# Performance work log

Hardware: AMD Instinct MI355X
Metric: run time of the kernel (lower is better)

## Reference

```python
import jax, jax.numpy as jnp
import numpy as np

B, T, D = 2, 2048, 2048
H, KVH, DH = 16, 4, 128
WINDOW = 1024
EPS = 1e-6
THETA = 10000.0

def _rmsnorm(x, eps=EPS):
    # RMSNorm over last dim, no affine (rmsnorm_weights=False)
    return x * jax.lax.rsqrt(jnp.mean(jnp.square(x), axis=-1, keepdims=True) + eps)

def _rope_tables(seq_len, dim, theta):
    inv_freq = 1.0 / theta ** (jnp.arange(0, dim, 2, dtype=jnp.float32) / dim)
    t = jnp.arange(seq_len, dtype=jnp.float32)
    freqs = jnp.outer(t, inv_freq)  # [T, dim//2]
    return jnp.cos(freqs), jnp.sin(freqs)

def _apply_rotary(x, cos, sin):
    # x: [B,T,H,DH]; cos/sin: [T, DH//2] broadcast to [1,T,1,DH//2]
    d = x.shape[-1] // 2
    x1, x2 = x[..., :d], x[..., d:]
    c = cos[None, :, None, :]
    s = sin[None, :, None, :]
    y1 = x1 * c + x2 * s
    y2 = -x1 * s + x2 * c
    return jnp.concatenate([y1, y2], axis=-1)

def setup_inputs() -> dict:
    key = jax.random.key(0)
    ks = jax.random.split(key, 5)
    sc = 0.02
    return {
        "hidden_states": jax.random.normal(ks[0], (B, T, D), dtype=jnp.float32),
        "Wq": jax.random.normal(ks[1], (D, H * DH), dtype=jnp.float32) * sc,
        "Wk": jax.random.normal(ks[2], (D, KVH * DH), dtype=jnp.float32) * sc,
        "Wv": jax.random.normal(ks[3], (D, KVH * DH), dtype=jnp.float32) * sc,
        "Wg": jax.random.normal(ks[4], (D, D), dtype=jnp.float32) * sc,
        "softmax_scaler": jnp.ones((H,), dtype=jnp.float32),
        "gn_weight": jnp.ones((DH,), dtype=jnp.float32),
    }

def reference(hidden_states, Wq, Wk, Wv, Wg, softmax_scaler, gn_weight):
    x = hidden_states
    b, t, _ = x.shape
    q = (x @ Wq).reshape(b, t, H, DH)
    k = (x @ Wk).reshape(b, t, KVH, DH)
    v = (x @ Wv).reshape(b, t, KVH, DH)

    # per-head QK RMSNorm
    q = _rmsnorm(q)
    k = _rmsnorm(k)

    # RoPE (local / swa branch, base=rope_theta_local)
    cos, sin = _rope_tables(t, DH, THETA)
    q = _apply_rotary(q, cos, sin)
    k = _apply_rotary(k, cos, sin)

    # scalable softmax: scale q by learned per-head scaler * log(position+1)
    log_pos = jnp.log(jnp.arange(1, t + 1, dtype=jnp.float32))  # [T]
    q = q * (softmax_scaler[None, None, :, None] * log_pos[None, :, None, None])

    # GQA: repeat kv heads (each kv head -> n_rep consecutive q heads)
    n_rep = H // KVH
    k = jnp.repeat(k, n_rep, axis=2)  # [B,T,H,DH]
    v = jnp.repeat(v, n_rep, axis=2)

    # causal + sliding-window attention (flash window_size=(w,w) causal => q-k in [0, w])
    scale = 1.0 / jnp.sqrt(jnp.float32(DH))
    scores = jnp.einsum("bqhd,bkhd->bhqk", q, k) * scale  # [B,H,T,T]
    qi = jnp.arange(t)[:, None]
    ki = jnp.arange(t)[None, :]
    mask = (ki <= qi) & (qi - ki <= WINDOW)  # [T,T]
    scores = jnp.where(mask[None, None, :, :], scores, jnp.float32(-1e30))
    p = jax.nn.softmax(scores, axis=-1)
    y = jnp.einsum("bhqk,bkhd->bqhd", p, v)  # [B,T,H,DH]

    # gate (elementwise, silu) then group RMSNorm (norm_before_gate_attn=False)
    g = (x @ Wg).reshape(b, t, H, DH)
    y = y * jax.nn.silu(g)
    y = _rmsnorm(y) * gn_weight  # groupnorm: RMSNorm over d_head with weight

    return y.reshape(b, t, D)
```

## Files before the change

### kernel.cpp

```cpp
#include <hip/hip_runtime.h>

#define B_   2
#define T_   2048
#define D_   2048
#define H_   16
#define KVH_ 4
#define DH_  128
#define WIN_ 1024
#define N_TOT 5120

typedef __attribute__((ext_vector_type(4))) float    f32x4;
typedef __attribute__((ext_vector_type(8))) _Float16 half8;
typedef __attribute__((ext_vector_type(8))) short    short8;
typedef __attribute__((ext_vector_type(4))) short    short4v;

__device__ __forceinline__ unsigned short f2h(float f) {
    _Float16 h = (_Float16)f;
    return __builtin_bit_cast(unsigned short, h);
}

__device__ __forceinline__ f32x4 mfma16x16x32(short8 a, short8 b, f32x4 c) {
    return __builtin_amdgcn_mfma_f32_16x16x32_f16(
        __builtin_bit_cast(half8, a), __builtin_bit_cast(half8, b), c, 0, 0, 0);
}

__device__ __forceinline__ void glds16(const void* g, void* l) {
    __builtin_amdgcn_global_load_lds(
        (const __attribute__((address_space(1))) unsigned int*)g,
        (__attribute__((address_space(3))) unsigned int*)l, 16, 0, 0);
}

__global__ void rope_tab_kernel(float* __restrict__ cosT, float* __restrict__ sinT) {
    int idx = blockIdx.x * 256 + threadIdx.x;
    if (idx >= T_ * 64) return;
    int t = idx >> 6, i = idx & 63;
    float inv = powf(10000.0f, -(float)i / 64.0f);
    float f = (float)t * inv;
    cosT[idx] = cosf(f);
    sinT[idx] = sinf(f);
}

__global__ void xconv_kernel(const float* __restrict__ xf, unsigned short* __restrict__ xb) {
    int idx = blockIdx.x * 256 + threadIdx.x;
    float4 f0 = ((const float4*)xf)[idx * 2];
    float4 f1 = ((const float4*)xf)[idx * 2 + 1];
    unsigned p0 = f2h(f0.x) | ((unsigned)f2h(f0.y) << 16);
    unsigned p1 = f2h(f0.z) | ((unsigned)f2h(f0.w) << 16);
    unsigned p2 = f2h(f1.x) | ((unsigned)f2h(f1.y) << 16);
    unsigned p3 = f2h(f1.z) | ((unsigned)f2h(f1.w) << 16);
    ((uint4*)xb)[idx] = make_uint4(p0, p1, p2, p3);
}

__global__ __launch_bounds__(256) void wtconv_kernel(
    const float* __restrict__ W, unsigned short* __restrict__ WTdst, int nW) {
    __shared__ unsigned short tile[64][72];
    int ntiles_n = nW >> 6;
    int n0 = (blockIdx.x % ntiles_n) * 64;
    int k0 = (blockIdx.x / ntiles_n) * 64;
    int tid = threadIdx.x;
    {
        int kr = tid >> 2, c0 = (tid & 3) * 16;
        const float* src = W + (size_t)(k0 + kr) * nW + n0 + c0;
        float4 a = ((const float4*)src)[0], b = ((const float4*)src)[1];
        float4 c = ((const float4*)src)[2], d = ((const float4*)src)[3];
        uint4 lo = make_uint4(f2h(a.x) | ((unsigned)f2h(a.y) << 16),
                              f2h(a.z) | ((unsigned)f2h(a.w) << 16),
                              f2h(b.x) | ((unsigned)f2h(b.y) << 16),
                              f2h(b.z) | ((unsigned)f2h(b.w) << 16));
        uint4 hi = make_uint4(f2h(c.x) | ((unsigned)f2h(c.y) << 16),
                              f2h(c.z) | ((unsigned)f2h(c.w) << 16),
                              f2h(d.x) | ((unsigned)f2h(d.y) << 16),
                              f2h(d.z) | ((unsigned)f2h(d.w) << 16));
        *(uint4*)(&tile[kr][c0])     = lo;
        *(uint4*)(&tile[kr][c0 + 8]) = hi;
    }
    __syncthreads();
    {
        int nr = tid >> 2, kc = (tid & 3) * 16;
        unsigned short vals[16];
        #pragma unroll
        for (int j = 0; j < 16; ++j) vals[j] = tile[kc + j][nr];
        uint4 lo = *(uint4*)(&vals[0]);
        uint4 hi = *(uint4*)(&vals[8]);
        unsigned short* dst = WTdst + (size_t)(n0 + nr) * D_ + k0 + kc;
        *(uint4*)(dst)     = lo;
        *(uint4*)(dst + 8) = hi;
    }
}

__global__ __launch_bounds__(256) void gemm_bt_kernel(
    const unsigned short* __restrict__ Ab, const unsigned short* __restrict__ Bt,
    float* __restrict__ C) {
    __shared__ unsigned short As[128 * 64];
    __shared__ unsigned short Bs[128 * 64];
    const int tid = threadIdx.x;
    const int l = tid & 63, w = tid >> 6;
    const int wr = w >> 1, wc = w & 1;
    int swz = (blockIdx.x & 7) * 160 + (blockIdx.x >> 3);
    const int mb0 = (swz / 40) * 128, nb0 = (swz % 40) * 128;

    f32x4 acc[4][4] = {};

    for (int k0 = 0; k0 < D_; k0 += 64) {
        __syncthreads();
        #pragma unroll
        for (int r = 0; r < 4; ++r) {
            int idx = r * 256 + tid;
            int m = idx >> 3, u = idx & 7;
            glds16(Ab + (size_t)(mb0 + m) * D_ + k0 + u * 8, &As[idx * 8]);
            glds16(Bt + (size_t)(nb0 + m) * D_ + k0 + u * 8, &Bs[idx * 8]);
        }
        __syncthreads();
        #pragma unroll
        for (int ks = 0; ks < 2; ++ks) {
            short8 af[4], bfr[4];
            #pragma unroll
            for (int mi = 0; mi < 4; ++mi)
                af[mi] = *(const short8*)(&As[(wr * 64 + mi * 16 + (l & 15)) * 64 + ks * 32 + (l >> 4) * 8]);
            #pragma unroll
            for (int ni = 0; ni < 4; ++ni)
                bfr[ni] = *(const short8*)(&Bs[(wc * 64 + ni * 16 + (l & 15)) * 64 + ks * 32 + (l >> 4) * 8]);
            #pragma unroll
            for (int mi = 0; mi < 4; ++mi)
                #pragma unroll
                for (int ni = 0; ni < 4; ++ni)
                    acc[mi][ni] = mfma16x16x32(af[mi], bfr[ni], acc[mi][ni]);
        }
    }
    #pragma unroll
    for (int mi = 0; mi < 4; ++mi)
        #pragma unroll
        for (int ni = 0; ni < 4; ++ni)
            #pragma unroll
            for (int i = 0; i < 4; ++i)
                C[(size_t)(mb0 + wr * 64 + mi * 16 + (l >> 4) * 4 + i) * N_TOT
                  + nb0 + wc * 64 + ni * 16 + (l & 15)] = acc[mi][ni][i];
}

__global__ __launch_bounds__(256) void qk_post_kernel(
    const float* __restrict__ C, int colofs, unsigned short* __restrict__ dst,
    const float* __restrict__ cosT, const float* __restrict__ sinT,
    const float* __restrict__ sscale, int nheads, int is_q) {
    int rid = blockIdx.x * 4 + (threadIdx.x >> 6);
    int lane = threadIdx.x & 63;
    int h = rid % nheads;
    int t = (rid / nheads) % T_;
    int b = rid / (nheads * T_);
    const float* row = C + (size_t)(b * T_ + t) * N_TOT + colofs + h * 128;
    float x1 = row[lane], x2 = row[lane + 64];
    float ss = x1 * x1 + x2 * x2;
    #pragma unroll
    for (int m = 1; m < 64; m <<= 1) ss += __shfl_xor(ss, m);
    float rn = rsqrtf(ss * (1.0f / 128.0f) + 1e-6f);
    float c = cosT[t * 64 + lane], s = sinT[t * 64 + lane];
    float y1 = x1 * c + x2 * s;
    float y2 = x2 * c - x1 * s;
    float sc = rn;
    if (is_q) sc *= sscale[h] * logf((float)(t + 1)) * 0.08838834764831845f;
    y1 *= sc; y2 *= sc;
    unsigned short* drow = dst + ((size_t)(b * nheads + h) * T_ + t) * 128;
    drow[lane]      = f2h(y1);
    drow[lane + 64] = f2h(y2);
}

__global__ void vconv_kernel(const float* __restrict__ C, unsigned short* __restrict__ vb) {
    int idx = blockIdx.x * 256 + threadIdx.x;
    int c8  = idx & 15;
    int kvh = (idx >> 4) & 3;
    int t   = (idx >> 6) & 2047;
    int b   = idx >> 17;
    const float* src = C + (size_t)(b * T_ + t) * N_TOT + 2560 + kvh * 128 + c8 * 8;
    float4 f0 = ((const float4*)src)[0];
    float4 f1 = ((const float4*)src)[1];
    unsigned p0 = f2h(f0.x) | ((unsigned)f2h(f0.y) << 16);
    unsigned p1 = f2h(f0.z) | ((unsigned)f2h(f0.w) << 16);
    unsigned p2 = f2h(f1.x) | ((unsigned)f2h(f1.y) << 16);
    unsigned p3 = f2h(f1.z) | ((unsigned)f2h(f1.w) << 16);
    unsigned short* dst = vb + ((size_t)(b * KVH_ + kvh) * T_ + t) * 128 + c8 * 8;
    *(uint4*)dst = make_uint4(p0, p1, p2, p3);
}

__global__ __launch_bounds__(256) void attn_kernel(
    const unsigned short* __restrict__ Q, const unsigned short* __restrict__ K,
    const unsigned short* __restrict__ V, float* __restrict__ O) {
    __shared__ __align__(16) char smem[34816];
    unsigned short* Kl = (unsigned short*)smem;
    unsigned short* Vt = (unsigned short*)smem + 64 * 136;

    const int tid = threadIdx.x, l = tid & 63, w = tid >> 6;
    const int qbi = blockIdx.x & 31, h = (blockIdx.x >> 5) & 15, b = blockIdx.x >> 9;
    const int qb = qbi * 64, kvh = h >> 2;
    const unsigned short* Qp = Q + (size_t)(b * H_ + h) * T_ * 128;
    const unsigned short* Kp = K + (size_t)(b * KVH_ + kvh) * T_ * 128;
    const unsigned short* Vp = V + (size_t)(b * KVH_ + kvh) * T_ * 128;
    const int qw = qb + w * 16;
    const int qi = qw + (l & 15);

    short8 qfr[4];
    #pragma unroll
    for (int dk = 0; dk < 4; ++dk)
        qfr[dk] = *(const short8*)(Qp + (size_t)(qw + (l & 15)) * 128 + dk * 32 + (l >> 4) * 8);

    f32x4 Oa[8] = {};
    float mrun = -1e30f, lrun = 0.0f;

    const int k0 = (qb - WIN_ > 0) ? (qb - WIN_) : 0;
    for (int tile = k0; tile <= qb; tile += 64) {
        __syncthreads();
        #pragma unroll
        for (int r = 0; r < 4; ++r) {
            int uidx = tid + 256 * r;
            int key = uidx >> 4, u = uidx & 15;
            int4 val = *(const int4*)(Kp + (size_t)(tile + key) * 128 + u * 8);
            int byte = (key * 256 + u * 16) ^ ((key & 7) << 4);
            *(int4*)((char*)Kl + byte) = val;
        }
        {
            int kb = tid >> 4, db = tid & 15;
            unsigned short vr[4][8];
            #pragma unroll
            for (int ki = 0; ki < 4; ++ki)
                *(int4*)vr[ki] = *(const int4*)(Vp + (size_t)(tile + kb * 4 + ki) * 128 + db * 8);
            #pragma unroll
            for (int di = 0; di < 8; ++di) {
                unsigned lo = vr[0][di] | ((unsigned)vr[1][di] << 16);
                unsigned hi = vr[2][di] | ((unsigned)vr[3][di] << 16);
                *(uint2*)(&Vt[(db * 8 + di) * 68 + kb * 4]) = make_uint2(lo, hi);
            }
        }
        __syncthreads();

        #pragma unroll
        for (int pair = 0; pair < 2; ++pair) {
            int kp = tile + pair * 32;
            if (kp > qw + 15) continue;
            if (kp + 31 < qw - WIN_) continue;

            f32x4 s0 = {}, s1 = {};
            __builtin_amdgcn_s_setprio(1);
            #pragma unroll
            for (int dk = 0; dk < 4; ++dk) {
                int r0 = pair * 32 + (l & 15), r1 = r0 + 16;
                int c  = dk * 64 + (l >> 4) * 16;
                short8 kf0 = *(const short8*)((char*)Kl + ((r0 * 256 + c) ^ ((r0 & 7) << 4)));
                short8 kf1 = *(const short8*)((char*)Kl + ((r1 * 256 + c) ^ ((r1 & 7) << 4)));
                s0 = mfma16x16x32(kf0, qfr[dk], s0);
                s1 = mfma16x16x32(kf1, qfr[dk], s1);
            }
            __builtin_amdgcn_s_setprio(0);
            float smax = -1e30f;
            #pragma unroll
            for (int i = 0; i < 4; ++i) {
                int ki0 = kp + (l >> 4) * 4 + i;
                int ki1 = ki0 + 16;
                if (ki0 > qi || qi - ki0 > WIN_) s0[i] = -1e30f;
                if (ki1 > qi || qi - ki1 > WIN_) s1[i] = -1e30f;
                smax = fmaxf(smax, fmaxf(s0[i], s1[i]));
            }
            smax = fmaxf(smax, __shfl_xor(smax, 16));
            smax = fmaxf(smax, __shfl_xor(smax, 32));
            if (!__all(smax <= mrun + 8.0f)) {
                float mnew = fmaxf(mrun, smax);
                float alpha = __expf(mrun - mnew);
                lrun *= alpha;
                #pragma unroll
                for (int dt = 0; dt < 8; ++dt) Oa[dt] *= alpha;
                mrun = mnew;
            }
            float psum = 0.0f;
            short8 pb;
            #pragma unroll
            for (int i = 0; i < 4; ++i) {
                float p0 = __expf(s0[i] - mrun);
                float p1 = __expf(s1[i] - mrun);
                psum += p0 + p1;
                pb[i]     = (short)f2h(p0);
                pb[i + 4] = (short)f2h(p1);
            }
            psum += __shfl_xor(psum, 16);
            psum += __shfl_xor(psum, 32);
            lrun += psum;
            __builtin_amdgcn_s_setprio(1);
            #pragma unroll
            for (int dt = 0; dt < 8; ++dt) {
                union { short4v hlf[2]; short8 v8; } vu;
                vu.hlf[0] = *(const short4v*)(&Vt[(dt * 16 + (l & 15)) * 68 + pair * 32 +      (l >> 4) * 4]);
                vu.hlf[1] = *(const short4v*)(&Vt[(dt * 16 + (l & 15)) * 68 + pair * 32 + 16 + (l >> 4) * 4]);
                Oa[dt] = mfma16x16x32(vu.v8, pb, Oa[dt]);
            }
            __builtin_amdgcn_s_setprio(0);
        }
    }

    __syncthreads();
    float* Ow = (float*)smem + w * (16 * 132);
    float inv = 1.0f / lrun;
    #pragma unroll
    for (int dt = 0; dt < 8; ++dt)
        #pragma unroll
        for (int i = 0; i < 4; ++i)
            Ow[(l & 15) * 132 + dt * 16 + (l >> 4) * 4 + i] = Oa[dt][i] * inv;
    #pragma unroll
    for (int j = 0; j < 8; ++j) {
        int idx4 = l + 64 * j;
        int row = idx4 >> 5, dpos = (idx4 & 31) * 4;
        float4 val = *(const float4*)(&Ow[row * 132 + dpos]);
        *(float4*)(O + ((size_t)(b * H_ + h) * T_ + qw + row) * 128 + dpos) = val;
    }
}

__global__ __launch_bounds__(256) void gate_norm_kernel(
    const float* __restrict__ o, const float* __restrict__ C,
    const float* __restrict__ gnw, float* __restrict__ out) {
    int rid = blockIdx.x * 4 + (threadIdx.x >> 6);
    int lane = threadIdx.x & 63;
    int h = rid & 15;
    int t = (rid >> 4) & 2047;
    int b = rid >> 15;
    const float* orow = o + ((size_t)(b * H_ + h) * T_ + t) * 128;
    const float* grow = C + (size_t)(b * T_ + t) * N_TOT + 3072 + h * 128;
    float o1 = orow[lane], o2 = orow[lane + 64];
    float g1 = grow[lane], g2 = grow[lane + 64];
    float y1 = o1 * (g1 / (1.0f + __expf(-g1)));
    float y2 = o2 * (g2 / (1.0f + __expf(-g2)));
    float ss = y1 * y1 + y2 * y2;
    #pragma unroll
    for (int m = 1; m < 64; m <<= 1) ss += __shfl_xor(ss, m);
    float rn = rsqrtf(ss * (1.0f / 128.0f) + 1e-6f);
    float* wrow = out + (size_t)rid * 128;
    wrow[lane]      = y1 * rn * gnw[lane];
    wrow[lane + 64] = y2 * rn * gnw[lane + 64];
}

extern "C" void kernel_launch(void* const* d_in, const int* in_sizes, int n_in,
                              void* d_out, int out_size, void* d_ws, size_t ws_size,
                              hipStream_t stream) {
    const float* x      = (const float*)d_in[0];
    const float* Wq     = (const float*)d_in[1];
    const float* Wk     = (const float*)d_in[2];
    const float* Wv     = (const float*)d_in[3];
    const float* Wg     = (const float*)d_in[4];
    const float* sscale = (const float*)d_in[5];
    const float* gnw    = (const float*)d_in[6];
    float* out = (float*)d_out;

    char* ws = (char*)d_ws;
    unsigned short* xh16 = (unsigned short*)(ws);
    unsigned short* WT   = (unsigned short*)(ws + 16777216);
    float*          C    = (float*)(ws + 37748736);
    unsigned short* qh16 = (unsigned short*)(ws + 121634816);
    unsigned short* kh16 = (unsigned short*)(ws + 138412032);
    unsigned short* vh16 = (unsigned short*)(ws + 142606336);
    float*          cosT = (float*)(ws + 146800640);
    float*          sinT = (float*)(ws + 147324928);
    float*          o    = (float*)(ws);

    rope_tab_kernel<<<512, 256, 0, stream>>>(cosT, sinT);

    xconv_kernel<<<4096, 256, 0, stream>>>(x, xh16);
    wtconv_kernel<<<1024, 256, 0, stream>>>(Wq, WT,                       2048);
    wtconv_kernel<<<256,  256, 0, stream>>>(Wk, WT + (size_t)2048 * D_,   512);
    wtconv_kernel<<<256,  256, 0, stream>>>(Wv, WT + (size_t)2560 * D_,   512);
    wtconv_kernel<<<1024, 256, 0, stream>>>(Wg, WT + (size_t)3072 * D_,   2048);

    gemm_bt_kernel<<<1280, 256, 0, stream>>>(xh16, WT, C);

    qk_post_kernel<<<16384, 256, 0, stream>>>(C, 0,    qh16, cosT, sinT, sscale, H_,   1);
    qk_post_kernel<<<4096,  256, 0, stream>>>(C, 2048, kh16, cosT, sinT, sscale, KVH_, 0);
    vconv_kernel<<<1024, 256, 0, stream>>>(C, vh16);

    attn_kernel<<<B_ * H_ * (T_ / 64), 256, 0, stream>>>(qh16, kh16, vh16, o);

    gate_norm_kernel<<<16384, 256, 0, stream>>>(o, C, gnw, out);
}
```

Measured before the change: 425.1 us.

## Replace fused QKVG GEMM with 256x256 tile, 8-wave double-buffered pipelined kernel

Rewrites the projection GEMM to use 256x256 output tiles with 8 waves per block, split-K LDS staging into double-buffered halves, and explicit interleaving of global-to-LDS prefetch with MFMA clusters using sched/s_barrier and vmcnt waits. The aim is to raise data reuse per loaded tile and hide global-load latency behind matrix math, cutting the GEMM's share of total time. The cost is 128 KB of LDS per block and a larger accumulator register footprint. There are also only 320 blocks for 256 CUs, which may leave a partial wave tail.

Result: faster. 413.0 us (-2.9%).

```diff
diff --git a/kernel.cpp b/kernel.cpp
--- a/kernel.cpp
+++ b/kernel.cpp
@@ -88,53 +88,104 @@
     }
 }
 
-__global__ __launch_bounds__(256) void gemm_bt_kernel(
+#define LDSOFF(d,s,kh) ((((d)*2+(s))*2+(kh))*8192)
+#define LDA_(d,qk,mf) (*(const short8*)(&ldsbuf[LDSOFF(d,0,qk) + (wm*128 + (mf)*16 + lr)*32 + lg*8]))
+#define LDB_(d,qk,nf) (*(const short8*)(&ldsbuf[LDSOFF(d,1,qk) + (wn*64  + (nf)*16 + lr)*32 + lg*8]))
+#define STAGE(d,s,kh,tile,base,R0) do { \
+    _Pragma("unroll") \
+    for (int ll = 0; ll < 2; ++ll) { \
+      int c_ = ll*512 + tid; \
+      int rr_ = c_ >> 2, sl_ = c_ & 3; \
+      glds16((base) + (size_t)((R0) + rr_) * D_ + (tile)*64 + (kh)*32 + sl_*8, \
+             &ldsbuf[LDSOFF(d,s,kh) + c_*8]); \
+    } \
+  } while (0)
+#define SBAR do { __builtin_amdgcn_sched_barrier(0); __builtin_amdgcn_s_barrier(); } while (0)
+#define MFMA_CLUSTER(QN2) do { \
+    __builtin_amdgcn_s_setprio(1); \
+    _Pragma("unroll") \
+    for (int mf = 0; mf < 8; ++mf) { \
+      acc[mf][(QN2)*2]   = mfma16x16x32(af[mf], bf0, acc[mf][(QN2)*2]); \
+      acc[mf][(QN2)*2+1] = mfma16x16x32(af[mf], bf1, acc[mf][(QN2)*2+1]); \
+    } \
+    __builtin_amdgcn_s_setprio(0); \
+  } while (0)
+
+__global__ __launch_bounds__(512, 2) void gemm8_kernel(
     const unsigned short* __restrict__ Ab, const unsigned short* __restrict__ Bt,
     float* __restrict__ C) {
-    __shared__ unsigned short As[128 * 64];
-    __shared__ unsigned short Bs[128 * 64];
+    __shared__ unsigned short ldsbuf[65536];
     const int tid = threadIdx.x;
-    const int l = tid & 63, w = tid >> 6;
-    const int wr = w >> 1, wc = w & 1;
-    int swz = (blockIdx.x & 7) * 160 + (blockIdx.x >> 3);
-    const int mb0 = (swz / 40) * 128, nb0 = (swz % 40) * 128;
-
-    f32x4 acc[4][4] = {};
-
-    for (int k0 = 0; k0 < D_; k0 += 64) {
-        __syncthreads();
-        #pragma unroll
-        for (int r = 0; r < 4; ++r) {
-            int idx = r * 256 + tid;
-            int m = idx >> 3, u = idx & 7;
-            glds16(Ab + (size_t)(mb0 + m) * D_ + k0 + u * 8, &As[idx * 8]);
-            glds16(Bt + (size_t)(nb0 + m) * D_ + k0 + u * 8, &Bs[idx * 8]);
-        }
-        __syncthreads();
-        #pragma unroll
-        for (int ks = 0; ks < 2; ++ks) {
-            short8 af[4], bfr[4];
-            #pragma unroll
-            for (int mi = 0; mi < 4; ++mi)
-                af[mi] = *(const short8*)(&As[(wr * 64 + mi * 16 + (l & 15)) * 64 + ks * 32 + (l >> 4) * 8]);
-            #pragma unroll
-            for (int ni = 0; ni < 4; ++ni)
-                bfr[ni] = *(const short8*)(&Bs[(wc * 64 + ni * 16 + (l & 15)) * 64 + ks * 32 + (l >> 4) * 8]);
-            #pragma unroll
-            for (int mi = 0; mi < 4; ++mi)
-                #pragma unroll
-                for (int ni = 0; ni < 4; ++ni)
-                    acc[mi][ni] = mfma16x16x32(af[mi], bfr[ni], acc[mi][ni]);
-        }
+    const int lr = tid & 15, lg = (tid >> 4) & 3;
+    const int wid = tid >> 6;
+    const int wm = wid >> 2, wn = wid & 3;
+    int swz = (blockIdx.x & 7) * 40 + (blockIdx.x >> 3);
+    const int MB0 = (swz / 20) * 256, NB0 = (swz % 20) * 256;
+
+    f32x4 acc[8][4] = {};
+
+    STAGE(0,0,0, 0, Ab, MB0);  STAGE(0,1,0, 0, Bt, NB0);
+    STAGE(0,0,1, 0, Ab, MB0);  STAGE(0,1,1, 0, Bt, NB0);
+    STAGE(1,0,0, 1, Ab, MB0);  STAGE(1,1,0, 1, Bt, NB0);
+    STAGE(1,0,1, 1, Ab, MB0);  STAGE(1,1,1, 1, Bt, NB0);
+    asm volatile("s_waitcnt vmcnt(8)" ::: "memory");
+    __builtin_amdgcn_s_barrier();
+
+    for (int j = 0; j < 16; ++j) {
+        const int tO = 2*j + 1;
+        const bool sP = (j >= 1);
+        const bool sN = (j < 15);
+        short8 af[8], bf0, bf1;
+        #pragma unroll
+        for (int mf = 0; mf < 8; ++mf) af[mf] = LDA_(0,0,mf);
+        bf0 = LDB_(0,0,0); bf1 = LDB_(0,0,1);
+        if (sP) STAGE(1,0,1, tO, Ab, MB0);
+        SBAR; MFMA_CLUSTER(0); SBAR;
+        bf0 = LDB_(0,0,2); bf1 = LDB_(0,0,3);
+        if (sP) STAGE(1,1,1, tO, Bt, NB0);
+        SBAR; MFMA_CLUSTER(1); SBAR;
+        #pragma unroll
+        for (int mf = 0; mf < 8; ++mf) af[mf] = LDA_(0,1,mf);
+        bf0 = LDB_(0,1,0); bf1 = LDB_(0,1,1);
+        if (sN) STAGE(0,0,0, 2*j+2, Ab, MB0);
+        SBAR; MFMA_CLUSTER(0); SBAR;
+        bf0 = LDB_(0,1,2); bf1 = LDB_(0,1,3);
+        if (sN) STAGE(0,1,0, 2*j+2, Bt, NB0);
+        __builtin_amdgcn_sched_barrier(0); __builtin_amdgcn_s_barrier();
+        MFMA_CLUSTER(1);
+        if (sN) asm volatile("s_waitcnt vmcnt(4)" ::: "memory");
+        else    asm volatile("s_waitcnt vmcnt(0)" ::: "memory");
+        SBAR;
+        #pragma unroll
+        for (int mf = 0; mf < 8; ++mf) af[mf] = LDA_(1,0,mf);
+        bf0 = LDB_(1,0,0); bf1 = LDB_(1,0,1);
+        if (sN) STAGE(0,0,1, 2*j+2, Ab, MB0);
+        SBAR; MFMA_CLUSTER(0); SBAR;
+        bf0 = LDB_(1,0,2); bf1 = LDB_(1,0,3);
+        if (sN) STAGE(0,1,1, 2*j+2, Bt, NB0);
+        SBAR; MFMA_CLUSTER(1); SBAR;
+        #pragma unroll
+        for (int mf = 0; mf < 8; ++mf) af[mf] = LDA_(1,1,mf);
+        bf0 = LDB_(1,1,0); bf1 = LDB_(1,1,1);
+        if (sN) STAGE(1,0,0, 2*j+3, Ab, MB0);
+        SBAR; MFMA_CLUSTER(0); SBAR;
+        bf0 = LDB_(1,1,2); bf1 = LDB_(1,1,3);
+        if (sN) STAGE(1,1,0, 2*j+3, Bt, NB0);
+        __builtin_amdgcn_sched_barrier(0); __builtin_amdgcn_s_barrier();
+        MFMA_CLUSTER(1);
+        if (sN) asm volatile("s_waitcnt vmcnt(4)" ::: "memory");
+        else    asm volatile("s_waitcnt vmcnt(0)" ::: "memory");
+        SBAR;
     }
-    #pragma unroll
-    for (int mi = 0; mi < 4; ++mi)
-        #pragma unroll
-        for (int ni = 0; ni < 4; ++ni)
+
+    #pragma unroll
+    for (int mf = 0; mf < 8; ++mf)
+        #pragma unroll
+        for (int nf = 0; nf < 4; ++nf)
             #pragma unroll
             for (int i = 0; i < 4; ++i)
-                C[(size_t)(mb0 + wr * 64 + mi * 16 + (l >> 4) * 4 + i) * N_TOT
-                  + nb0 + wc * 64 + ni * 16 + (l & 15)] = acc[mi][ni][i];
+                C[(size_t)(MB0 + wm*128 + mf*16 + lg*4 + i) * N_TOT
+                  + NB0 + wn*64 + nf*16 + lr] = acc[mf][nf][i];
 }
 
 __global__ __launch_bounds__(256) void qk_post_kernel(
@@ -363,7 +414,7 @@
     wtconv_kernel<<<256,  256, 0, stream>>>(Wv, WT + (size_t)2560 * D_,   512);
     wtconv_kernel<<<1024, 256, 0, stream>>>(Wg, WT + (size_t)3072 * D_,   2048);
 
-    gemm_bt_kernel<<<1280, 256, 0, stream>>>(xh16, WT, C);
+    gemm8_kernel<<<320, 512, 0, stream>>>(xh16, WT, C);
 
     qk_post_kernel<<<16384, 256, 0, stream>>>(C, 0,    qh16, cosT, sinT, sscale, H_,   1);
     qk_post_kernel<<<4096,  256, 0, stream>>>(C, 2048, kh16, cosT, sinT, sscale, KVH_, 0);
```
